# Kernel tuning notes

Hardware: AMD Instinct MI355X
Metric: run time of the kernel (lower is better)

The kernel has to match this reference:

```python
import jax, jax.numpy as jnp
from jax import lax
import numpy as np


def conv2d(x, w, b=None, padding=0, dilation=1, groups=1):
    out = lax.conv_general_dilated(
        x, w, window_strides=(1, 1),
        padding=[(padding, padding), (padding, padding)],
        rhs_dilation=(dilation, dilation),
        dimension_numbers=('NCHW', 'OIHW', 'NCHW'),
        feature_group_count=groups)
    return out if b is None else out + b[None, :, None, None]


def hardswish(x):
    return x * jnp.clip(x + 3.0, 0.0, 6.0) / 6.0


def leaky(x, s):
    return jnp.where(x >= 0, x, s * x)


def bn_eval(x, g, b, eps=1e-5):
    # BatchNorm2d eval mode with running_mean=0, running_var=1
    scale = g * (1.0 / float(np.sqrt(1.0 + eps)))
    return x * scale[None, :, None, None] + b[None, :, None, None]


def deform_dw_conv(x, offset, w):
    # torchvision DeformConv2d, depthwise (groups=C), k=3, stride=1, pad=1, dil=1
    # x [B,C,H,W], offset [B,18,H,W] (y,x interleaved, kernel row-major), w [C,1,3,3]
    B, C, H, W = x.shape
    xf = x.reshape(B, C, H * W)
    yy = jnp.arange(H, dtype=x.dtype)[:, None]
    xx = jnp.arange(W, dtype=x.dtype)[None, :]
    out = jnp.zeros_like(x)
    for k in range(9):
        ky, kx = k // 3 - 1, k % 3 - 1
        py = yy + ky + offset[:, 2 * k]          # [B,H,W]
        px = xx + kx + offset[:, 2 * k + 1]
        y0 = jnp.floor(py)
        x0 = jnp.floor(px)
        wy = py - y0
        wx = px - x0
        y0i = y0.astype(jnp.int32)
        x0i = x0.astype(jnp.int32)
        val = jnp.zeros_like(x)
        for dy, dx, wgt in ((0, 0, (1 - wy) * (1 - wx)), (0, 1, (1 - wy) * wx),
                            (1, 0, wy * (1 - wx)), (1, 1, wy * wx)):
            iy = y0i + dy
            ix = x0i + dx
            valid = (iy >= 0) & (iy < H) & (ix >= 0) & (ix < W)
            idx = (jnp.clip(iy, 0, H - 1) * W + jnp.clip(ix, 0, W - 1)).reshape(B, 1, H * W)
            g = jnp.take_along_axis(xf, idx, axis=2).reshape(B, C, H, W)
            val = val + g * (wgt * valid.astype(x.dtype))[:, None]
        out = out + val * w[:, 0, ky + 1, kx + 1][None, :, None, None]
    return out


def patch_embed(x, off_dw, off_pw, dcn_w, pw_w):
    g = x.shape[1]
    off = conv2d(x, off_dw, padding=1, groups=g)
    off = jnp.clip(conv2d(off, off_pw), -1.0, 1.0)
    y = deform_dw_conv(x, off, dcn_w)
    return hardswish(conv2d(y, pw_w))


def depth_conv(x, dw_w, dw_b, pw_w, pw_b):
    g = x.shape[1]
    return conv2d(conv2d(x, dw_w, dw_b, padding=1, groups=g), pw_w, pw_b)


def cross_attn(hs, ctx, dw_w, dw_b, pw_w, pw_b):
    q = depth_conv(hs, dw_w[0], dw_b[0], pw_w[0], pw_b[0])
    k = depth_conv(ctx, dw_w[1], dw_b[1], pw_w[1], pw_b[1])
    v = depth_conv(ctx, dw_w[2], dw_b[2], pw_w[2], pw_b[2])
    head = q.shape[1] // 8  # num_heads = 8
    qt = q.transpose(0, 2, 1, 3)  # [B,H,C,W]
    kt = k.transpose(0, 2, 1, 3)
    vt = v.transpose(0, 2, 1, 3)
    scores = jnp.einsum('bhcw,bhdw->bhcd', qt, kt) / float(np.sqrt(head))
    probs = jax.nn.softmax(scores, axis=-1)
    o = jnp.einsum('bhcd,bhdw->bhcw', probs, vt)
    return o.transpose(0, 2, 1, 3)  # back to [B,C,H,W]


def dilated_block(x, ws, bs):
    h = x
    for i, d in enumerate((1, 2, 3, 2, 1)):
        h = conv2d(h, ws[i], bs[i], padding=d, dilation=d)
        if i < 4:
            h = leaky(h, 0.01)
    return h + x


def fft_block(h, fd1_w, fd2_w, fd1_g, fd1_bt, fd2_g, fd2_bt, fconv_w):
    Hh, Ww = h.shape[-2], h.shape[-1]
    xf = jnp.fft.rfft2(h)  # norm='backward'
    re, im = jnp.real(xf), jnp.imag(xf)
    mag = jnp.sqrt(re * re + im * im)
    pha = jnp.arctan2(im, re)

    def branch(m, i):
        t = leaky(bn_eval(conv2d(m, fd1_w[i]), fd1_g[i], fd1_bt[i]), 0.1)
        m1 = jnp.concatenate([m, t], 1)          # C+32
        t2 = leaky(bn_eval(conv2d(m1, fd2_w[i]), fd2_g[i], fd2_bt[i]), 0.1)
        m2 = jnp.concatenate([m1, t2], 1)        # C+64
        return conv2d(m2, fconv_w[i])            # back to C

    mag_o = branch(mag, 0)
    pha_o = branch(pha, 1)
    real = mag_o * jnp.cos(pha_o)
    imag = mag_o * jnp.sin(pha_o)
    out = jnp.fft.irfft2(lax.complex(real, imag), s=(Hh, Ww)) + h
    return out, mag_o, pha_o


def scarm_forward(x, ch_off_dw, ch_off_pw, ch_dcn_w, ch_pw,
                  ct_off_dw, ct_off_pw, ct_dcn_w, ct_pw,
                  db_w, db_b, ca_dw_w, ca_dw_b, ca_pw_w, ca_pw_b,
                  convHH_w, convHH_b, fd1_w, fd2_w, fd1_g, fd1_bt,
                  fd2_g, fd2_bt, fconv_w, conv_w, conv_b):
    b = x.shape[0]
    residual = x
    h = patch_embed(x, ch_off_dw, ch_off_pw, ch_dcn_w, ch_pw)  # [B,64,H,W]
    fft_out, mag, pha = fft_block(h, fd1_w, fd2_w, fd1_g, fd1_bt, fd2_g, fd2_bt, fconv_w)
    t = b // 3
    x_HL, x_LH, x_HH = h[:t], h[t:2 * t], h[2 * t:]
    # note: faithful to source, which aliases fft_LH/fft_HH back to x (h)
    fft_HL, fft_LH, fft_HH = fft_out[:t], h[t:2 * t], h[2 * t:]
    x_HH_LH = cross_attn(x_LH, x_HH, ca_dw_w[0], ca_dw_b[0], ca_pw_w[0], ca_pw_b[0])
    x_HH_HL = cross_attn(x_HL, x_HH, ca_dw_w[1], ca_dw_b[1], ca_pw_w[1], ca_pw_b[1])
    f_HH_LH = cross_attn(fft_LH, fft_HH, ca_dw_w[0], ca_dw_b[0], ca_pw_w[0], ca_pw_b[0])
    f_HH_HL = cross_attn(fft_HL, fft_HH, ca_dw_w[1], ca_dw_b[1], ca_pw_w[1], ca_pw_b[1])
    x_HL2 = dilated_block(x_HL, db_w[1], db_b[1])
    x_LH2 = dilated_block(x_LH, db_w[0], db_b[0])
    x_HH2 = dilated_block(conv2d(jnp.concatenate([x_HH_LH, x_HH_HL], 1), convHH_w, convHH_b, padding=1), db_w[2], db_b[2])
    f_HH2 = dilated_block(conv2d(jnp.concatenate([f_HH_LH, f_HH_HL], 1), convHH_w, convHH_b, padding=1), db_w[2], db_b[2])
    out = patch_embed(jnp.concatenate([x_HL2, x_LH2, x_HH2], 0), ct_off_dw, ct_off_pw, ct_dcn_w, ct_pw)
    fftout = patch_embed(jnp.concatenate([fft_HL, fft_LH, f_HH2], 0), ct_off_dw, ct_off_pw, ct_dcn_w, ct_pw)
    out = conv2d(jnp.concatenate([out, fftout], 1), conv_w, conv_b, padding=1)
    return out + residual, mag, pha


def setup_inputs() -> dict:
    key = jax.random.key(0)
    ks = iter(jax.random.split(key, 32))

    def rn(shape, scale):
        return jax.random.normal(next(ks), shape, jnp.float32) * scale

    return {
        'x': rn([12, 3, 128, 128], 1.0),
        'ch_off_dw': rn([3, 1, 3, 3], 0.3), 'ch_off_pw': rn([18, 3, 1, 1], 0.3),
        'ch_dcn_w': rn([3, 1, 3, 3], 0.3), 'ch_pw': rn([64, 3, 1, 1], 0.3),
        'ct_off_dw': rn([64, 1, 3, 3], 0.1), 'ct_off_pw': rn([18, 64, 1, 1], 0.1),
        'ct_dcn_w': rn([64, 1, 3, 3], 0.1), 'ct_pw': rn([3, 64, 1, 1], 0.05),
        'db_w': rn([3, 5, 64, 64, 3, 3], 0.05), 'db_b': rn([3, 5, 64], 0.01),
        'ca_dw_w': rn([2, 3, 64, 1, 3, 3], 0.3), 'ca_dw_b': rn([2, 3, 64], 0.01),
        'ca_pw_w': rn([2, 3, 64, 64, 1, 1], 0.1), 'ca_pw_b': rn([2, 3, 64], 0.01),
        'convHH_w': rn([64, 128, 3, 3], 0.03), 'convHH_b': rn([64], 0.01),
        'fd1_w': rn([2, 32, 64, 1, 1], 0.1), 'fd2_w': rn([2, 32, 96, 1, 1], 0.1),
        'fd1_g': 1.0 + rn([2, 32], 0.1), 'fd1_bt': rn([2, 32], 0.1),
        'fd2_g': 1.0 + rn([2, 32], 0.1), 'fd2_bt': rn([2, 32], 0.1),
        'fconv_w': rn([2, 64, 128, 1, 1], 0.1),
        'conv_w': rn([3, 6, 3, 3], 0.1), 'conv_b': rn([3], 0.01),
    }


def reference(x, ch_off_dw, ch_off_pw, ch_dcn_w, ch_pw,
              ct_off_dw, ct_off_pw, ct_dcn_w, ct_pw,
              db_w, db_b, ca_dw_w, ca_dw_b, ca_pw_w, ca_pw_b,
              convHH_w, convHH_b, fd1_w, fd2_w, fd1_g, fd1_bt,
              fd2_g, fd2_bt, fconv_w, conv_w, conv_b):
    return scarm_forward(x, ch_off_dw, ch_off_pw, ch_dcn_w, ch_pw,
                         ct_off_dw, ct_off_pw, ct_dcn_w, ct_pw,
                         db_w, db_b, ca_dw_w, ca_dw_b, ca_pw_w, ca_pw_b,
                         convHH_w, convHH_b, fd1_w, fd2_w, fd1_g, fd1_bt,
                         fd2_g, fd2_bt, fconv_w, conv_w, conv_b)
```

## Files before the change

kernel.cpp:

```cpp
#include <hip/hip_runtime.h>

namespace {

constexpr int Hn = 128, Wn = 128, HWn = 16384, HWFn = 8320;
constexpr float TWOPI = 6.2831853071795864769f;
constexpr float BN_SCALE = 0.99999500003749968f;

typedef __attribute__((ext_vector_type(8))) short short8;
typedef __attribute__((ext_vector_type(4))) float float4v;

__device__ __forceinline__ short f2bf(float v){
  unsigned u = __float_as_uint(v);
  u += 0x7FFF + ((u >> 16) & 1);
  return (short)(u >> 16);
}
__device__ __forceinline__ float bf2f(unsigned short u){
  return __uint_as_float(((unsigned)u) << 16);
}

__global__ void k_pack(const float* __restrict__ w, unsigned short* __restrict__ o,
                       int Cin, int csz, int n){
  int idx = blockIdx.x*256 + threadIdx.x;
  if (idx >= n) return;
  int ck = idx / csz;
  int i  = idx - ck*csz;
  const float* wp = w + (size_t)ck*csz;
  int j = i & 7, lane = (i>>3)&63, mt = (i>>9)&3, p = i>>11;
  int blk = p/18, r = p - blk*18, tap = r>>1, ks = r&1;
  int co = mt*16 + (lane & 15);
  int ci = blk*64 + ks*32 + ((lane>>4)<<3) + j;
  o[idx] = (unsigned short)f2bf(wp[((size_t)co*Cin + ci)*9 + tap]);
}

__global__ void k_packpw(const float* __restrict__ w, unsigned short* __restrict__ o,
                         int Cout, int MT, int n){
  int i = blockIdx.x*256 + threadIdx.x;
  if (i >= n) return;
  int per = MT << 10;
  int set = i / per;
  int r = i - set*per;
  int j = r & 7, lane = (r>>3)&63, blk = r>>9;
  int ks = blk / MT, mt = blk - ks*MT;
  int co = mt*16 + (lane & 15);
  int ci = ks*32 + ((lane>>4)<<3) + j;
  float v = (co < Cout) ? w[(size_t)set*Cout*64 + co*64 + ci] : 0.f;
  o[i] = (unsigned short)f2bf(v);
}

__global__ void k_wfdc(const float* __restrict__ fd1w, const float* __restrict__ fd2w,
                       const float* __restrict__ fcw,  const float* __restrict__ fd1g,
                       const float* __restrict__ fd2g, float* __restrict__ o){
  int i = blockIdx.x*256 + threadIdx.x;
  if (i >= 26624) return;
  int br = i / 13312, r = i - br*13312;
  float v;
  if (r < 2048){
    int ci = r >> 5, j = r & 31;
    v = fd1w[br*2048 + j*64 + ci] * (fd1g[br*32 + j]*BN_SCALE);
  } else if (r < 5120){
    int rr = r - 2048; int ci = rr >> 5, j = rr & 31;
    v = fd2w[br*3072 + j*96 + ci] * (fd2g[br*32 + j]*BN_SCALE);
  } else {
    int rr = r - 5120; int ci = rr >> 6, j = rr & 63;
    v = fcw[br*8192 + j*128 + ci];
  }
  o[i] = v;
}

__global__ __launch_bounds__(256) void k_fdc(
    const float* __restrict__ in, const float* __restrict__ wT,
    const float* __restrict__ bt1, const float* __restrict__ bt2,
    float* __restrict__ outp){
  __shared__ float tls[32][64];
  __shared__ float uls[32][64];
  int b = blockIdx.x, tile = blockIdx.y;
  int tid = threadIdx.x;
  int lane = tid & 63;
  int kk = __builtin_amdgcn_readfirstlane(tid >> 6);
  const float* ip = in + (size_t)b*64*HWFn + tile*64 + lane;
  {
    float t[8];
    #pragma unroll
    for (int jj=0;jj<8;jj++) t[jj] = bt1[kk*8+jj];
    for (int ci=0; ci<64; ci++){
      float v = ip[(size_t)ci*HWFn];
      const float* w = wT + ci*32 + kk*8;
      #pragma unroll
      for (int jj=0;jj<8;jj++) t[jj] = fmaf(v, w[jj], t[jj]);
    }
    #pragma unroll
    for (int jj=0;jj<8;jj++){
      float a = t[jj];
      tls[kk*8+jj][lane] = (a>=0.f)? a : 0.1f*a;
    }
  }
  __syncthreads();
  {
    float u[8];
    #pragma unroll
    for (int jj=0;jj<8;jj++) u[jj] = bt2[kk*8+jj];
    for (int ci=0; ci<64; ci++){
      float v = ip[(size_t)ci*HWFn];
      const float* w = wT + 2048 + ci*32 + kk*8;
      #pragma unroll
      for (int jj=0;jj<8;jj++) u[jj] = fmaf(v, w[jj], u[jj]);
    }
    for (int ci=0; ci<32; ci++){
      float v = tls[ci][lane];
      const float* w = wT + 2048 + (64+ci)*32 + kk*8;
      #pragma unroll
      for (int jj=0;jj<8;jj++) u[jj] = fmaf(v, w[jj], u[jj]);
    }
    #pragma unroll
    for (int jj=0;jj<8;jj++){
      float a = u[jj];
      uls[kk*8+jj][lane] = (a>=0.f)? a : 0.1f*a;
    }
  }
  __syncthreads();
  float acc[16];
  #pragma unroll
  for (int jj=0;jj<16;jj++) acc[jj] = 0.f;
  for (int ci=0; ci<64; ci++){
    float v = ip[(size_t)ci*HWFn];
    const float* w = wT + 5120 + ci*64 + kk*16;
    #pragma unroll
    for (int jj=0;jj<16;jj++) acc[jj] = fmaf(v, w[jj], acc[jj]);
  }
  for (int ci=0; ci<32; ci++){
    float v = tls[ci][lane];
    const float* w = wT + 5120 + (64+ci)*64 + kk*16;
    #pragma unroll
    for (int jj=0;jj<16;jj++) acc[jj] = fmaf(v, w[jj], acc[jj]);
  }
  for (int ci=0; ci<32; ci++){
    float v = uls[ci][lane];
    const float* w = wT + 5120 + (96+ci)*64 + kk*16;
    #pragma unroll
    for (int jj=0;jj<16;jj++) acc[jj] = fmaf(v, w[jj], acc[jj]);
  }
  float* op = outp + (size_t)b*64*HWFn + tile*64 + lane;
  #pragma unroll
  for (int jj=0;jj<16;jj++)
    op[(size_t)(kk*16+jj)*HWFn] = acc[jj];
}

constexpr int XST = 72;
__global__ __launch_bounds__(256) void k_mconv(
    const float* __restrict__ in, const float* __restrict__ in2,
    const unsigned short* __restrict__ wpk, const float* __restrict__ bias,
    const float* __restrict__ res, float* __restrict__ out,
    int nblk, int dl, int leaky){
  __shared__ short lds[3*134*XST];
  int b = blockIdx.x >> 7, y = blockIdx.x & 127;
  int tid = threadIdx.x;
  int wv = tid >> 6, lane = tid & 63;
  int nq = lane >> 4, nr = lane & 15;
  float4v acc[4][2];
  #pragma unroll
  for (int mt=0; mt<4; mt++)
    #pragma unroll
    for (int nt=0; nt<2; nt++) acc[mt][nt] = (float4v){0.f,0.f,0.f,0.f};

  for (int blk=0; blk<nblk; blk++){
    const float* src = blk ? in2 : in;
    __syncthreads();
    for (int e = tid; e < 3*16*32; e += 256){
      int dy = e >> 9;
      int r  = e & 511;
      int c4 = r >> 5;
      int xx = (r & 31) << 2;
      int yy = y + (dy-1)*dl;
      float4 v0, v1, v2, v3;
      if (yy >= 0 && yy < Hn){
        const float* sp2 = src + (((size_t)b*64 + c4*4)*Hn + yy)*Wn + xx;
        v0 = *(const float4*)(sp2);
        v1 = *(const float4*)(sp2 + HWn);
        v2 = *(const float4*)(sp2 + 2*HWn);
        v3 = *(const float4*)(sp2 + 3*HWn);
      } else {
        v0 = v1 = v2 = v3 = make_float4(0.f,0.f,0.f,0.f);
      }
      #pragma unroll
      for (int j=0; j<4; j++){
        float f0 = (&v0.x)[j], f1 = (&v1.x)[j], f2 = (&v2.x)[j], f3 = (&v3.x)[j];
        unsigned p0 = ((unsigned)(unsigned short)f2bf(f0)) | (((unsigned)(unsigned short)f2bf(f1)) << 16);
        unsigned p1 = ((unsigned)(unsigned short)f2bf(f2)) | (((unsigned)(unsigned short)f2bf(f3)) << 16);
        *(uint2*)&lds[(dy*134 + xx + 3 + j)*XST + c4*4] = make_uint2(p0, p1);
      }
    }
    for (int e = tid; e < 3*16*6; e += 256){
      int dy = e / 96; int r = e - dy*96;
      int c4 = r / 6;  int k = r - c4*6;
      int x = (k < 3) ? k : 128 + k;
      *(uint2*)&lds[(dy*134 + x)*XST + c4*4] = make_uint2(0u, 0u);
    }
    __syncthreads();
    const unsigned short* wb = wpk + (size_t)blk*36864;
    #pragma unroll 3
    for (int tap=0; tap<9; tap++){
      int dy = tap/3, dx = tap - (tap/3)*3;
      #pragma unroll
      for (int ks=0; ks<2; ks++){
        short8 a[4];
        #pragma unroll
        for (int mt=0; mt<4; mt++)
          a[mt] = *(const short8*)(wb + (((size_t)(tap*2+ks)*4+mt)<<9) + ((size_t)lane<<3));
        #pragma unroll
        for (int nt=0; nt<2; nt++){
          int x = wv*32 + nt*16 + nr + (dx-1)*dl + 3;
          short8 bf = *(const short8*)&lds[(dy*134 + x)*XST + ks*32 + nq*8];
          #pragma unroll
          for (int mt=0; mt<4; mt++)
            acc[mt][nt] = __builtin_amdgcn_mfma_f32_16x16x32_bf16(a[mt], bf, acc[mt][nt], 0, 0, 0);
        }
      }
    }
  }
  #pragma unroll
  for (int mt=0; mt<4; mt++)
  #pragma unroll
  for (int nt=0; nt<2; nt++){
    int x = wv*32 + nt*16 + nr;
    #pragma unroll
    for (int r2=0; r2<4; r2++){
      int co = mt*16 + nq*4 + r2;
      float a = acc[mt][nt][r2] + (bias ? bias[co] : 0.f);
      if (leaky) a = (a >= 0.f) ? a : 0.01f*a;
      size_t idx = (((size_t)b*64 + co)*Hn + y)*Wn + x;
      if (res) a += res[idx];
      out[idx] = a;
    }
  }
}

template<int MT>
__global__ __launch_bounds__(256) void k_dwpw(
    const float* __restrict__ in, const float* __restrict__ dww, const float* __restrict__ dwb,
    const unsigned short* __restrict__ pwpk, const float* __restrict__ pwb,
    float* __restrict__ out, int Cout, size_t outb, int post){
  __shared__ short tb[128*72];
  __shared__ float wsm[640];
  int b = blockIdx.x >> 7, y = blockIdx.x & 127;
  int tid = threadIdx.x;
  for (int i = tid; i < 640; i += 256)
    wsm[i] = (i < 576) ? dww[i] : (dwb ? dwb[i-576] : 0.f);
  __syncthreads();
  for (int e = tid; e < 2048; e += 256){
    int ci = e >> 5;
    int xx = (e & 31) << 2;
    const float* ip = in + ((size_t)b*64 + ci)*HWn;
    const float* wp = wsm + ci*9;
    float4 a0 = make_float4(0.f,0.f,0.f,0.f), a1 = a0, a2 = a0;
    float L0=0.f,L1=0.f,L2=0.f,R0=0.f,R1=0.f,R2=0.f;
    if (y > 0){
      const float* r = ip + (y-1)*Wn;
      a0 = *(const float4*)(r + xx);
      if (xx) L0 = r[xx-1];
      if (xx < 124) R0 = r[xx+4];
    }
    {
      const float* r = ip + y*Wn;
      a1 = *(const float4*)(r + xx);
      if (xx) L1 = r[xx-1];
      if (xx < 124) R1 = r[xx+4];
    }
    if (y < Hn-1){
      const float* r = ip + (y+1)*Wn;
      a2 = *(const float4*)(r + xx);
      if (xx) L2 = r[xx-1];
      if (xx < 124) R2 = r[xx+4];
    }
    float bb = wsm[576+ci];
    float o0=bb,o1=bb,o2=bb,o3=bb;
    float w0=wp[0],w1=wp[1],w2=wp[2];
    o0 = fmaf(w0,L0,  fmaf(w1,a0.x, fmaf(w2,a0.y, o0)));
    o1 = fmaf(w0,a0.x,fmaf(w1,a0.y, fmaf(w2,a0.z, o1)));
    o2 = fmaf(w0,a0.y,fmaf(w1,a0.z, fmaf(w2,a0.w, o2)));
    o3 = fmaf(w0,a0.z,fmaf(w1,a0.w, fmaf(w2,R0,   o3)));
    w0=wp[3];w1=wp[4];w2=wp[5];
    o0 = fmaf(w0,L1,  fmaf(w1,a1.x, fmaf(w2,a1.y, o0)));
    o1 = fmaf(w0,a1.x,fmaf(w1,a1.y, fmaf(w2,a1.z, o1)));
    o2 = fmaf(w0,a1.y,fmaf(w1,a1.z, fmaf(w2,a1.w, o2)));
    o3 = fmaf(w0,a1.z,fmaf(w1,a1.w, fmaf(w2,R1,   o3)));
    w0=wp[6];w1=wp[7];w2=wp[8];
    o0 = fmaf(w0,L2,  fmaf(w1,a2.x, fmaf(w2,a2.y, o0)));
    o1 = fmaf(w0,a2.x,fmaf(w1,a2.y, fmaf(w2,a2.z, o1)));
    o2 = fmaf(w0,a2.y,fmaf(w1,a2.z, fmaf(w2,a2.w, o2)));
    o3 = fmaf(w0,a2.z,fmaf(w1,a2.w, fmaf(w2,R2,   o3)));
    short* d = &tb[xx*72 + ci];
    d[0]   = f2bf(o0);
    d[72]  = f2bf(o1);
    d[144] = f2bf(o2);
    d[216] = f2bf(o3);
  }
  __syncthreads();
  int wv = tid>>6, lane = tid&63, nq = lane>>4, nr = lane&15;
  float4v acc[MT][2];
  #pragma unroll
  for (int mt=0; mt<MT; mt++)
    #pragma unroll
    for (int nt=0; nt<2; nt++) acc[mt][nt] = (float4v){0.f,0.f,0.f,0.f};
  #pragma unroll
  for (int ks=0; ks<2; ks++){
    short8 a[MT];
    #pragma unroll
    for (int mt=0; mt<MT; mt++)
      a[mt] = *(const short8*)(pwpk + ((ks*MT+mt)<<9) + (lane<<3));
    #pragma unroll
    for (int nt=0; nt<2; nt++){
      int x = wv*32 + nt*16 + nr;
      short8 bf = *(const short8*)&tb[x*72 + ks*32 + nq*8];
      #pragma unroll
      for (int mt=0; mt<MT; mt++)
        acc[mt][nt] = __builtin_amdgcn_mfma_f32_16x16x32_bf16(a[mt], bf, acc[mt][nt], 0, 0, 0);
    }
  }
  #pragma unroll
  for (int mt=0; mt<MT; mt++)
  #pragma unroll
  for (int nt=0; nt<2; nt++){
    int x = wv*32 + nt*16 + nr;
    #pragma unroll
    for (int r2=0; r2<4; r2++){
      int co = mt*16 + nq*4 + r2;
      if (co < Cout){
        float a = acc[mt][nt][r2] + (pwb ? pwb[co] : 0.f);
        if (post == 1) a = fminf(fmaxf(a, -1.f), 1.f);
        else if (post == 2) a = a*fminf(fmaxf(a+3.f, 0.f), 6.f)*(1.f/6.f);
        out[(size_t)b*outb + (size_t)co*HWn + y*Wn + x] = a;
      }
    }
  }
}

__global__ __launch_bounds__(512) void k_defpw(
    const float* __restrict__ xg, const float* __restrict__ off, const float* __restrict__ dcnw,
    const unsigned short* __restrict__ pwpk, float* __restrict__ out,
    int Cout, size_t outb, int post){
  __shared__ unsigned short xs[5*64*130];
  __shared__ short tb[128*72];
  __shared__ float wsm[576];
  int b = blockIdx.x >> 7, y = blockIdx.x & 127;
  int tid = threadIdx.x;
  int px = tid & 127, sub = tid >> 7;
  for (int i = tid; i < 576; i += 512) wsm[i] = dcnw[i];
  for (int e = tid; e < 10240; e += 512){
    int tr = e >> 11;
    int r  = e & 2047;
    int ci = r >> 5;
    int xx = (r & 31) << 2;
    int gy = min(max(y - 2 + tr, 0), Hn-1);
    float4 v = *(const float4*)&xg[(((size_t)b*64 + ci)*Hn + gy)*Wn + xx];
    unsigned short* d = &xs[(tr*64 + ci)*130 + xx];
    d[0] = (unsigned short)f2bf(v.x);
    d[1] = (unsigned short)f2bf(v.y);
    d[2] = (unsigned short)f2bf(v.z);
    d[3] = (unsigned short)f2bf(v.w);
  }
  const float* op = off + (size_t)b*18*HWn + y*Wn + px;
  int t0[9], t1[9], c0[9], c1[9];
  float w00[9], w01[9], w10[9], w11[9];
  #pragma unroll
  for (int k=0; k<9; k++){
    int ky = k/3 - 1, kx = k - (k/3)*3 - 1;
    float oy = op[(size_t)(2*k)*HWn];
    float ox = op[(size_t)(2*k+1)*HWn];
    float py = (float)(y + ky) + oy;
    float pxx = (float)(px + kx) + ox;
    float fy = floorf(py), fx = floorf(pxx);
    float wy = py - fy, wx = pxx - fx;
    int y0 = (int)fy, x0 = (int)fx;
    float vy0 = (y0 >= 0 && y0 < Hn) ? 1.f : 0.f;
    float vy1 = (y0+1 >= 0 && y0+1 < Hn) ? 1.f : 0.f;
    float vx0 = (x0 >= 0 && x0 < Wn) ? 1.f : 0.f;
    float vx1 = (x0+1 >= 0 && x0+1 < Wn) ? 1.f : 0.f;
    w00[k] = (1.f-wy)*(1.f-wx)*vy0*vx0;
    w01[k] = (1.f-wy)*wx*vy0*vx1;
    w10[k] = wy*(1.f-wx)*vy1*vx0;
    w11[k] = wy*wx*vy1*vx1;
    t0[k] = min(max(min(max(y0,   0), Hn-1) - (y-2), 0), 4);
    t1[k] = min(max(min(max(y0+1, 0), Hn-1) - (y-2), 0), 4);
    c0[k] = min(max(x0,   0), Wn-1);
    c1[k] = min(max(x0+1, 0), Wn-1);
  }
  __syncthreads();
  for (int ci = sub; ci < 64; ci += 4){
    float acc = 0.f;
    #pragma unroll
    for (int k=0; k<9; k++){
      const unsigned short* b0 = &xs[(t0[k]*64 + ci)*130];
      const unsigned short* b1 = &xs[(t1[k]*64 + ci)*130];
      float v = w00[k]*bf2f(b0[c0[k]]) + w01[k]*bf2f(b0[c1[k]])
              + w10[k]*bf2f(b1[c0[k]]) + w11[k]*bf2f(b1[c1[k]]);
      acc = fmaf(v, wsm[ci*9 + k], acc);
    }
    tb[px*72 + ci] = f2bf(acc);
  }
  __syncthreads();
  int wv = tid>>6, lane = tid&63, nq = lane>>4, nr = lane&15;
  float4v acc = (float4v){0.f,0.f,0.f,0.f};
  int x = wv*16 + nr;
  #pragma unroll
  for (int ks=0; ks<2; ks++){
    short8 a = *(const short8*)(pwpk + (ks<<9) + (lane<<3));
    short8 bf = *(const short8*)&tb[x*72 + ks*32 + nq*8];
    acc = __builtin_amdgcn_mfma_f32_16x16x32_bf16(a, bf, acc, 0, 0, 0);
  }
  #pragma unroll
  for (int r2=0; r2<4; r2++){
    int co = nq*4 + r2;
    if (co < Cout){
      float a = acc[r2];
      if (post == 2) a = a*fminf(fmaxf(a+3.f, 0.f), 6.f)*(1.f/6.f);
      out[(size_t)b*outb + (size_t)co*HWn + y*Wn + x] = a;
    }
  }
}

__global__ void k_dw3x3(const float* __restrict__ in, const float* __restrict__ w,
                        const float* __restrict__ bias, float* __restrict__ out, int C){
  int bc = blockIdx.x; int y = blockIdx.y; int x = threadIdx.x;
  int c = bc % C;
  const float* ip = in + (size_t)bc*HWn;
  const float* wp = w + c*9;
  float acc = bias ? bias[c] : 0.f;
  #pragma unroll
  for (int ky=0; ky<3; ky++){
    int yy = y + ky - 1; if (yy < 0 || yy >= Hn) continue;
    #pragma unroll
    for (int kx=0; kx<3; kx++){
      int xx = x + kx - 1; if (xx < 0 || xx >= Wn) continue;
      acc = fmaf(ip[yy*Wn+xx], wp[ky*3+kx], acc);
    }
  }
  out[(size_t)bc*HWn + y*Wn + x] = acc;
}

template<int CT>
__global__ void k_pwt(const float* __restrict__ in, const float* __restrict__ wg,
                      const float* __restrict__ bias, const float* __restrict__ bng,
                      const float* __restrict__ bnb, float* __restrict__ out,
                      int Cin, int Cout, int npix, int inb, int outb, int post, float slope){
  extern __shared__ float wsm[];
  int nt = (Cout + CT - 1)/CT;
  int b = blockIdx.x / nt, t = blockIdx.x - b*nt;
  int co0 = t*CT;
  for (int i = threadIdx.x; i < CT*Cin; i += 256){
    int co = i / Cin;
    wsm[i] = (co0 + co < Cout) ? wg[(size_t)(co0+co)*Cin + (i - co*Cin)] : 0.f;
  }
  __syncthreads();
  int p = blockIdx.y*256 + threadIdx.x;
  if (p >= npix) return;
  const float* ip = in + (size_t)b*inb + p;
  float acc[CT];
  #pragma unroll
  for (int j=0; j<CT; j++) acc[j] = 0.f;
  for (int ci=0; ci<Cin; ci++){
    float v = ip[(size_t)ci*npix];
    #pragma unroll
    for (int j=0; j<CT; j++) acc[j] = fmaf(v, wsm[j*Cin+ci], acc[j]);
  }
  #pragma unroll
  for (int j=0; j<CT; j++){
    int co = co0 + j;
    if (co < Cout){
      float a = acc[j] + (bias ? bias[co] : 0.f);
      if (bng) a = a*(bng[co]*BN_SCALE) + bnb[co];
      if (post == 1) a = fminf(fmaxf(a, -1.f), 1.f);
      else if (post == 2) a = a*fminf(fmaxf(a+3.f, 0.f), 6.f)*(1.f/6.f);
      else if (post == 3) a = (a >= 0.f) ? a : a*slope;
      out[(size_t)b*outb + (size_t)co*npix + p] = a;
    }
  }
}

__global__ void k_deform(const float* __restrict__ x, const float* __restrict__ off,
                         const float* __restrict__ w, float* __restrict__ out, int C){
  int bc = blockIdx.x; int b = bc / C; int c = bc - b*C;
  int y = blockIdx.y; int x0 = threadIdx.x;
  const float* xp = x + (size_t)bc*HWn;
  const float* op = off + (size_t)b*18*HWn + y*Wn + x0;
  const float* wp = w + c*9;
  float acc = 0.f;
  #pragma unroll
  for (int k=0; k<9; k++){
    int ky = k/3 - 1, kx = k - (k/3)*3 - 1;
    float oy = op[(size_t)(2*k)*HWn];
    float ox = op[(size_t)(2*k+1)*HWn];
    float py = (float)y + (float)ky + oy;
    float px = (float)x0 + (float)kx + ox;
    float fy = floorf(py), fx = floorf(px);
    float wy = py - fy, wx = px - fx;
    int y0 = (int)fy, xx0 = (int)fx;
    float val = 0.f;
    #pragma unroll
    for (int dy=0; dy<2; dy++){
      int iy = y0 + dy; if (iy < 0 || iy >= Hn) continue;
      float wyv = dy ? wy : (1.f - wy);
      #pragma unroll
      for (int dx=0; dx<2; dx++){
        int ix = xx0 + dx; if (ix < 0 || ix >= Wn) continue;
        float wxv = dx ? wx : (1.f - wx);
        val = fmaf(xp[iy*Wn+ix], wyv*wxv, val);
      }
    }
    acc = fmaf(val, wp[k], acc);
  }
  out[(size_t)bc*HWn + y*Wn + x0] = acc;
}

__global__ void k_conv3x3s(const float* __restrict__ in, const float* __restrict__ wgt,
                           const float* __restrict__ bias, const float* __restrict__ res,
                           float* __restrict__ out, int Cin, int Cout){
  int g = blockIdx.x;
  int b = g / Cout; int o0 = g - b*Cout;
  int y = blockIdx.y, x = threadIdx.x;
  float acc = bias ? bias[o0] : 0.f;
  for (int ci=0; ci<Cin; ci++){
    const float* iip = in + ((size_t)b*Cin + ci)*HWn;
    const float* wp = wgt + ((size_t)o0*Cin + ci)*9;
    #pragma unroll
    for (int ky=0; ky<3; ky++){
      int yy = y + ky - 1; if (yy < 0 || yy >= Hn) continue;
      #pragma unroll
      for (int kx=0; kx<3; kx++){
        int xx = x + kx - 1; if (xx < 0 || xx >= Wn) continue;
        acc = fmaf(iip[yy*Wn+xx], wp[ky*3+kx], acc);
      }
    }
  }
  size_t idx = ((size_t)b*Cout + o0)*HWn + y*Wn + x;
  if (res) acc += res[idx];
  out[idx] = acc;
}

__global__ __launch_bounds__(256) void k_attn(
    const float* __restrict__ q, const float* __restrict__ k,
    const float* __restrict__ v, float* __restrict__ o){
  __shared__ float qs[64][129];
  __shared__ float ks[64][129];
  __shared__ float vs[64][129];
  __shared__ float ps[64][66];
  int bh = blockIdx.x; int b = bh >> 7, h = bh & 127;
  size_t base = ((size_t)b*64*128 + h)*128;
  int tid = threadIdx.x;
  for (int e = tid; e < 8192; e += 256){
    int c = e >> 7, w = e & 127;
    size_t g = base + (size_t)c*HWn + w;
    qs[c][w] = q[g]; ks[c][w] = k[g]; vs[c][w] = v[g];
  }
  __syncthreads();
  {
    int c0 = (tid >> 4) << 2, d0 = (tid & 15) << 2;
    float acc[4][4];
    #pragma unroll
    for (int a=0; a<4; a++)
      #pragma unroll
      for (int bb=0; bb<4; bb++) acc[a][bb] = 0.f;
    for (int i=0; i<128; i++){
      float qv[4], kv[4];
      #pragma unroll
      for (int a=0; a<4; a++){ qv[a] = qs[c0+a][i]; kv[a] = ks[d0+a][i]; }
      #pragma unroll
      for (int a=0; a<4; a++)
        #pragma unroll
        for (int bb=0; bb<4; bb++) acc[a][bb] = fmaf(qv[a], kv[bb], acc[a][bb]);
    }
    #pragma unroll
    for (int a=0; a<4; a++)
      #pragma unroll
      for (int bb=0; bb<4; bb++)
        ps[c0+a][d0+bb] = acc[a][bb] * 0.35355339059327373f;
  }
  __syncthreads();
  {
    int wv = tid >> 6, lane = tid & 63;
    for (int it=0; it<16; it++){
      int row = wv*16 + it;
      float vv = ps[row][lane];
      float m = vv;
      #pragma unroll
      for (int off=32; off; off>>=1) m = fmaxf(m, __shfl_xor(m, off));
      float e = expf(vv - m);
      float s = e;
      #pragma unroll
      for (int off=32; off; off>>=1) s += __shfl_xor(s, off);
      ps[row][lane] = e / s;
    }
  }
  __syncthreads();
  {
    int c0 = (tid >> 4) << 2, w0 = (tid & 15) << 3;
    float acc[4][8];
    #pragma unroll
    for (int a=0; a<4; a++)
      #pragma unroll
      for (int j=0; j<8; j++) acc[a][j] = 0.f;
    for (int d=0; d<64; d++){
      float pv[4], vv[8];
      #pragma unroll
      for (int a=0; a<4; a++) pv[a] = ps[c0+a][d];
      #pragma unroll
      for (int j=0; j<8; j++) vv[j] = vs[d][w0+j];
      #pragma unroll
      for (int a=0; a<4; a++)
        #pragma unroll
        for (int j=0; j<8; j++) acc[a][j] = fmaf(pv[a], vv[j], acc[a][j]);
    }
    #pragma unroll
    for (int a=0; a<4; a++)
      #pragma unroll
      for (int j=0; j<8; j++)
        o[base + (size_t)(c0+a)*HWn + w0 + j] = acc[a][j];
  }
}

__device__ __forceinline__ float2 cmul(float2 a, float2 b){
  return make_float2(a.x*b.x - a.y*b.y, a.x*b.y + a.y*b.x);
}

__device__ __forceinline__ void wfft4(float2* z, const float2* twl, int l){
  #pragma unroll
  for (int q=0; q<2; q++){
    float dx = z[2*q].x - z[2*q+1].x, dy = z[2*q].y - z[2*q+1].y;
    z[2*q].x += z[2*q+1].x; z[2*q].y += z[2*q+1].y;
    z[2*q+1] = cmul(make_float2(dx, dy), twl[6]);
  }
  #pragma unroll
  for (int s = 5; s >= 0; --s){
    int h = 1 << s;
    bool up = (l & h) != 0;
    float2 w = twl[s];
    #pragma unroll
    for (int q=0; q<4; q++){
      float ox = __shfl_xor(z[q].x, h), oy = __shfl_xor(z[q].y, h);
      float sx = up ? ox - z[q].x : z[q].x + ox;
      float sy = up ? oy - z[q].y : z[q].y + oy;
      float2 t = cmul(make_float2(sx, sy), w);
      z[q].x = up ? t.x : sx;  z[q].y = up ? t.y : sy;
    }
  }
}

__device__ __forceinline__ void wreorder(float2 z0, float2 z1, float2& n0, float2& n1, int l){
  int a = (int)(__brev((unsigned)(l >> 1)) >> 26);
  float p0x = __shfl(z0.x, a),   p0y = __shfl(z0.y, a);
  float p1x = __shfl(z1.x, a),   p1y = __shfl(z1.y, a);
  float q0x = __shfl(z0.x, a+1), q0y = __shfl(z0.y, a+1);
  float q1x = __shfl(z1.x, a+1), q1y = __shfl(z1.y, a+1);
  bool odd = (l & 1) != 0;
  n0 = odd ? make_float2(p1x, p1y) : make_float2(p0x, p0y);
  n1 = odd ? make_float2(q1x, q1y) : make_float2(q0x, q0y);
}

__global__ __launch_bounds__(256) void k_fft2(
    const float* __restrict__ x, float* __restrict__ mag, float* __restrict__ pha){
  __shared__ float spr[8320];
  __shared__ float spi[8320];
  int img = blockIdx.x;
  int tid = threadIdx.x;
  int wv = tid >> 6, l = tid & 63;
  float2 twl[7];
  #pragma unroll
  for (int s = 0; s < 7; ++s){
    int jh = (l & ((1 << s) - 1)) << (6 - s);
    float sv, cv; sincosf(-TWOPI * (float)jh * (1.f/128.f), &sv, &cv);
    twl[s] = make_float2(cv, sv);
  }
  const float* xp = x + (size_t)img*HWn;
  for (int f = wv; f < 32; f += 4){
    int fB = f + 32;
    float2 z[4];
    {
      const float* a0 = xp + (2*f)*Wn;  const float* a1 = a0 + Wn;
      const float* b0 = xp + (2*fB)*Wn; const float* b1 = b0 + Wn;
      z[0] = make_float2(a0[l],      a1[l]);
      z[1] = make_float2(a0[64 + l], a1[64 + l]);
      z[2] = make_float2(b0[l],      b1[l]);
      z[3] = make_float2(b0[64 + l], b1[64 + l]);
    }
    wfft4(z, twl, l);
    #pragma unroll
    for (int q=0; q<2; q++){
      int ff = q ? fB : f;
      float2 n0, n1; wreorder(z[2*q], z[2*q+1], n0, n1, l);
      float zhx = __shfl(n1.x, (64 - l) & 63);
      float zhy = __shfl(n1.y, (64 - l) & 63);
      float2 Zn = (l == 0) ? n0 : make_float2(zhx, zhy);
      int iA = (2*ff)*65 + l, iB = (2*ff+1)*65 + l;
      spr[iA] = 0.5f*(n0.x + Zn.x);  spi[iA] = 0.5f*(n0.y - Zn.y);
      spr[iB] = 0.5f*(n0.y + Zn.y);  spi[iB] = 0.5f*(Zn.x - n0.x);
      if (l == 0){
        spr[(2*ff)*65 + 64]   = n1.x;  spi[(2*ff)*65 + 64]   = 0.f;
        spr[(2*ff+1)*65 + 64] = n1.y;  spi[(2*ff+1)*65 + 64] = 0.f;
      }
    }
  }
  __syncthreads();
  for (int c = wv; c < 33; c += 4){
    int cB = c + 33;
    bool h2 = cB < 65;
    int cB_s = h2 ? cB : c;
    float2 z[4];
    z[0] = make_float2(spr[l*65 + c],        spi[l*65 + c]);
    z[1] = make_float2(spr[(64 + l)*65 + c], spi[(64 + l)*65 + c]);
    z[2] = make_float2(spr[l*65 + cB_s],        spi[l*65 + cB_s]);
    z[3] = make_float2(spr[(64 + l)*65 + cB_s], spi[(64 + l)*65 + cB_s]);
    wfft4(z, twl, l);
    {
      float2 n0, n1; wreorder(z[0], z[1], n0, n1, l);
      spr[l*65 + c]        = sqrtf(n0.x*n0.x + n0.y*n0.y);
      spi[l*65 + c]        = atan2f(n0.y, n0.x);
      spr[(64 + l)*65 + c] = sqrtf(n1.x*n1.x + n1.y*n1.y);
      spi[(64 + l)*65 + c] = atan2f(n1.y, n1.x);
    }
    if (h2){
      float2 n0, n1; wreorder(z[2], z[3], n0, n1, l);
      spr[l*65 + cB]        = sqrtf(n0.x*n0.x + n0.y*n0.y);
      spi[l*65 + cB]        = atan2f(n0.y, n0.x);
      spr[(64 + l)*65 + cB] = sqrtf(n1.x*n1.x + n1.y*n1.y);
      spi[(64 + l)*65 + cB] = atan2f(n1.y, n1.x);
    }
  }
  __syncthreads();
  float* mp = mag + (size_t)img*HWFn;
  float* pp = pha + (size_t)img*HWFn;
  for (int i = tid; i < 8320; i += 256){
    mp[i] = spr[i]; pp[i] = spi[i];
  }
}

__global__ __launch_bounds__(256) void k_ifft2(
    const float* __restrict__ mo, const float* __restrict__ po,
    const float* __restrict__ hsrc, float* __restrict__ outp){
  __shared__ float spr[8320];
  __shared__ float spi[8320];
  int img = blockIdx.x;
  int tid = threadIdx.x;
  int wv = tid >> 6, l = tid & 63;
  float2 twl[7];
  #pragma unroll
  for (int s = 0; s < 7; ++s){
    int jh = (l & ((1 << s) - 1)) << (6 - s);
    float sv, cv; sincosf(TWOPI * (float)jh * (1.f/128.f), &sv, &cv);
    twl[s] = make_float2(cv, sv);
  }
  const float* mp = mo + (size_t)img*HWFn;
  const float* pp = po + (size_t)img*HWFn;
  for (int i = tid; i < 8320; i += 256){
    float m = mp[i], p = pp[i];
    float sv, cv; sincosf(p, &sv, &cv);
    spr[i] = m*cv; spi[i] = m*sv;
  }
  __syncthreads();
  for (int c = wv; c < 33; c += 4){
    int cB = c + 33;
    bool h2 = cB < 65;
    int cB_s = h2 ? cB : c;
    float2 z[4];
    z[0] = make_float2(spr[l*65 + c],        spi[l*65 + c]);
    z[1] = make_float2(spr[(64 + l)*65 + c], spi[(64 + l)*65 + c]);
    z[2] = make_float2(spr[l*65 + cB_s],        spi[l*65 + cB_s]);
    z[3] = make_float2(spr[(64 + l)*65 + cB_s], spi[(64 + l)*65 + cB_s]);
    wfft4(z, twl, l);
    {
      float2 n0, n1; wreorder(z[0], z[1], n0, n1, l);
      spr[l*65 + c] = n0.x;        spi[l*65 + c] = n0.y;
      spr[(64 + l)*65 + c] = n1.x; spi[(64 + l)*65 + c] = n1.y;
    }
    if (h2){
      float2 n0, n1; wreorder(z[2], z[3], n0, n1, l);
      spr[l*65 + cB] = n0.x;        spi[l*65 + cB] = n0.y;
      spr[(64 + l)*65 + cB] = n1.x; spi[(64 + l)*65 + cB] = n1.y;
    }
  }
  __syncthreads();
  const float scl = 1.f/16384.f;
  for (int f = wv; f < 32; f += 4){
    int fB = f + 32;
    float2 z[4];
    #pragma unroll
    for (int q=0; q<2; q++){
      int ff = q ? fB : f;
      int iA = (2*ff)*65 + l, iB = (2*ff+1)*65 + l;
      float2 A  = make_float2(spr[iA], spi[iA]);
      float2 Bv = make_float2(spr[iB], spi[iB]);
      if (l == 0){ A.y = 0.f; Bv.y = 0.f; }
      z[2*q] = make_float2(A.x - Bv.y, A.y + Bv.x);
      int lm = 64 - l;
      float2 Am = make_float2(spr[(2*ff)*65 + lm],   spi[(2*ff)*65 + lm]);
      float2 Bm = make_float2(spr[(2*ff+1)*65 + lm], spi[(2*ff+1)*65 + lm]);
      z[2*q+1] = (l == 0) ? make_float2(Am.x, Bm.x)
                          : make_float2(Am.x + Bm.y, Bm.x - Am.y);
    }
    wfft4(z, twl, l);
    #pragma unroll
    for (int q=0; q<2; q++){
      int ff = q ? fB : f;
      float2 n0, n1; wreorder(z[2*q], z[2*q+1], n0, n1, l);
      size_t g0 = (size_t)img*HWn + (size_t)(2*ff)*Wn + l;
      size_t g1 = g0 + Wn;
      outp[g0]      = n0.x*scl + hsrc[g0];
      outp[g0 + 64] = n1.x*scl + hsrc[g0 + 64];
      outp[g1]      = n0.y*scl + hsrc[g1];
      outp[g1 + 64] = n1.y*scl + hsrc[g1 + 64];
    }
  }
}

}

extern "C" void kernel_launch(void* const* d_in, const int* in_sizes, int n_in,
                              void* d_out, int out_size, void* d_ws, size_t ws_size,
                              hipStream_t stream){
  const float *xf   =(const float*)d_in[0],  *chodw=(const float*)d_in[1],
              *chopw=(const float*)d_in[2],  *chdcn=(const float*)d_in[3],
              *chpw =(const float*)d_in[4],  *ctodw=(const float*)d_in[5],
              *ctopw=(const float*)d_in[6],  *ctdcn=(const float*)d_in[7],
              *ctpw =(const float*)d_in[8],  *dbw  =(const float*)d_in[9],
              *dbb  =(const float*)d_in[10], *cadw =(const float*)d_in[11],
              *cadb =(const float*)d_in[12], *capw =(const float*)d_in[13],
              *capb =(const float*)d_in[14], *hhw  =(const float*)d_in[15],
              *hhb  =(const float*)d_in[16], *fd1w =(const float*)d_in[17],
              *fd2w =(const float*)d_in[18], *fd1g =(const float*)d_in[19],
              *fd1bt=(const float*)d_in[20], *fd2g =(const float*)d_in[21],
              *fd2bt=(const float*)d_in[22], *fcw  =(const float*)d_in[23],
              *cw   =(const float*)d_in[24], *cb   =(const float*)d_in[25];

  constexpr size_t M = 1048576;
  float* ws = (float*)d_ws;
  float* h     = ws;
  float* fftHL = ws + 12*M;
  float* cat6  = ws + 16*M;
  unsigned short* wpkDB = (unsigned short*)(cat6 + 1179648);
  unsigned short* wpkHH = wpkDB + 552960;
  float* wfdc = (float*)(wpkHH + 73728);
  float* P = cat6 + 1179648 + 313344 + 26624;

  const int NB = (ws_size >= 266018816ull) ? 4 : 1;
  const size_t S = (size_t)NB*M;
  float* kb  = P;        float* vb  = P + S;   float* qb  = P + 2*S;
  float* qsl = P + 3*S;
  float* aA  = P + 4*S;  float* aB  = P + 5*S;
  float* aC  = P + 6*S;  float* hh1 = P + 7*S; float* sA  = P + 8*S;
  float* sB  = P + 9*S;  float* dbuf= P + 10*S;
  float* X   = P + 11*S;
  unsigned short* pwpkCA = (unsigned short*)qsl;
  unsigned short* pwpkTO = pwpkCA + 24576;
  unsigned short* pwpkTP = pwpkTO + 2048;
  float* dwb3 = P; float* offb12 = P + 589824; float* yb3 = P + 4128768;

  float* out = (float*)d_out;
  float* out0 = out;
  float* out1 = out + 589824;
  float* out2 = out + 589824 + 6389760;

  auto PW = [&](const float* in, const float* wg, const float* bi, const float* g, const float* bt,
                float* o, int B, int Ci, int Co, int npix, int inb, int outb, int post, float slope){
    int py = (npix + 255)/256;
    if (Co > 32){
      k_pwt<32><<<dim3(B*2, py), 256, 32*Ci*4, stream>>>(in, wg, bi, g, bt, o, Ci, Co, npix, inb, outb, post, slope);
    } else if (Co > 18){
      k_pwt<32><<<dim3(B, py), 256, 32*Ci*4, stream>>>(in, wg, bi, g, bt, o, Ci, Co, npix, inb, outb, post, slope);
    } else if (Co > 3){
      k_pwt<18><<<dim3(B, py), 256, 18*Ci*4, stream>>>(in, wg, bi, g, bt, o, Ci, Co, npix, inb, outb, post, slope);
    } else {
      k_pwt<3><<<dim3(B, py), 256, 3*Ci*4, stream>>>(in, wg, bi, g, bt, o, Ci, Co, npix, inb, outb, post, slope);
    }
  };
  auto MCONV = [&](const float* in, const float* in2, const unsigned short* wp, const float* bi,
                   const float* res, float* o, int B, int nblk, int dl, int lk){
    k_mconv<<<B*128, 256, 0, stream>>>(in, in2, wp, bi, res, o, nblk, dl, lk);
  };
  auto DILm = [&](const float* in, int set, const float* bset, int B){
    const unsigned short* w5 = wpkDB + (size_t)set*5*36864;
    MCONV(in, nullptr, w5,          bset,      nullptr, sA,   B, 1, 1, 1);
    MCONV(sA, nullptr, w5+36864,    bset+64,   nullptr, sB,   B, 1, 2, 1);
    MCONV(sB, nullptr, w5+2*36864,  bset+128,  nullptr, sA,   B, 1, 3, 1);
    MCONV(sA, nullptr, w5+3*36864,  bset+192,  nullptr, sB,   B, 1, 2, 1);
    MCONV(sB, nullptr, w5+4*36864,  bset+256,  in,      dbuf, B, 1, 1, 0);
  };
  auto DCONVm = [&](const float* in, int idx, float* o, int B){
    k_dwpw<4><<<B*128, 256, 0, stream>>>(in, cadw + idx*576, cadb + idx*64,
        pwpkCA + (size_t)idx*4096, capb + idx*64, o, 64, (size_t)64*HWn, 0);
  };
  auto ATTNm = [&](const float* qsrc, int qidx, float* o, int B){
    DCONVm(qsrc, qidx, qb, B);
    k_attn<<<B*128, 256, 0, stream>>>(qb, kb, vb, o);
  };
  auto PEMBEDm = [&](const float* in, float* outSlice, int B){
    k_dwpw<2><<<B*128, 256, 0, stream>>>(in, ctodw, nullptr, pwpkTO, nullptr,
        X, 18, (size_t)18*HWn, 1);
    k_defpw<<<B*128, 512, 0, stream>>>(in, X, ctdcn, pwpkTP, outSlice, 3, (size_t)6*HWn, 2);
  };

  k_pack<<<(552960 + 255)/256, 256, 0, stream>>>(dbw, wpkDB, 64, 36864, 552960);
  k_pack<<<288, 256, 0, stream>>>(hhw, wpkHH, 128, 73728, 73728);
  k_wfdc<<<104, 256, 0, stream>>>(fd1w, fd2w, fcw, fd1g, fd2g, wfdc);

  k_dw3x3<<<dim3(36, Hn), 128, 0, stream>>>(xf, chodw, nullptr, dwb3, 3);
  PW(dwb3, chopw, nullptr, nullptr, nullptr, offb12, 12, 3, 18, HWn, 3*HWn, 18*HWn, 1, 0.f);
  k_deform<<<dim3(36, Hn), 128, 0, stream>>>(xf, offb12, chdcn, yb3, 3);
  PW(yb3, chpw, nullptr, nullptr, nullptr, h, 12, 3, 64, HWn, 3*HWn, 64*HWn, 2, 0.f);

  if (NB == 4){
    float* mB = P;
    float* pB = P + 6389760;
    k_fft2<<<768, 256, 0, stream>>>(h, mB, pB);
    k_fdc<<<dim3(12, 130), 256, 0, stream>>>(mB, wfdc,         fd1bt,      fd2bt,      out1);
    k_fdc<<<dim3(12, 130), 256, 0, stream>>>(pB, wfdc + 13312, fd1bt + 32, fd2bt + 32, out2);
    k_ifft2<<<256, 256, 0, stream>>>(out1, out2, h, fftHL);
  } else {
    float* mB = P;
    float* pB = P + 2129920;
    for (int c=0; c<3; c++){
      const float* hsrc = h + (size_t)c*4*M;
      float* o1 = out1 + (size_t)c*2129920;
      float* o2 = out2 + (size_t)c*2129920;
      k_fft2<<<256, 256, 0, stream>>>(hsrc, mB, pB);
      k_fdc<<<dim3(4, 130), 256, 0, stream>>>(mB, wfdc,         fd1bt,      fd2bt,      o1);
      k_fdc<<<dim3(4, 130), 256, 0, stream>>>(pB, wfdc + 13312, fd1bt + 32, fd2bt + 32, o2);
      if (c == 0)
        k_ifft2<<<256, 256, 0, stream>>>(out1, out2, h, fftHL);
    }
  }

  k_packpw<<<96, 256, 0, stream>>>(capw,  pwpkCA, 64, 4, 24576);
  k_packpw<<<8,  256, 0, stream>>>(ctopw, pwpkTO, 18, 2, 2048);
  k_packpw<<<4,  256, 0, stream>>>(ctpw,  pwpkTP, 3,  1, 1024);

  for (int g0=0; g0<4; g0+=NB){
    const float* hHL = h + (size_t)g0*M;
    const float* hLH = h + (size_t)(4+g0)*M;
    const float* hHH = h + (size_t)(8+g0)*M;
    const float* fHL = fftHL + (size_t)g0*M;
    DCONVm(hHH, 1, kb, NB);
    DCONVm(hHH, 2, vb, NB);
    ATTNm(hLH, 0, aA, NB);
    DCONVm(hHH, 4, kb, NB);
    DCONVm(hHH, 5, vb, NB);
    ATTNm(hHL, 3, aB, NB);
    ATTNm(fHL, 3, aC, NB);
    MCONV(aA, aB, wpkHH, hhb, nullptr, hh1, NB, 2, 1, 0);
    DILm(hh1, 2, dbb + 2*320, NB);
    PEMBEDm(dbuf, cat6 + (size_t)((8+g0)*6)*HWn, NB);
    MCONV(aA, aC, wpkHH, hhb, nullptr, hh1, NB, 2, 1, 0);
    DILm(hh1, 2, dbb + 2*320, NB);
    PEMBEDm(dbuf, cat6 + (size_t)((8+g0)*6+3)*HWn, NB);
    DILm(hHL, 1, dbb + 320, NB);
    PEMBEDm(dbuf, cat6 + (size_t)(g0*6)*HWn, NB);
    DILm(hLH, 0, dbb, NB);
    PEMBEDm(dbuf, cat6 + (size_t)((4+g0)*6)*HWn, NB);
    PEMBEDm(fHL, cat6 + (size_t)(g0*6+3)*HWn, NB);
    PEMBEDm(hLH, cat6 + (size_t)((4+g0)*6+3)*HWn, NB);
  }

  k_conv3x3s<<<dim3(36, Hn), 128, 0, stream>>>(cat6, cw, cb, xf, out0, 6, 3);
}
```

Measured before the change: 1.578 ms.

## Compute two dilated output rows per mconv block; widen FFT blocks to 512 threads

Result: slower. 1.675 ms (+6.1%).

```diff
diff --git a/kernel.cpp b/kernel.cpp
--- a/kernel.cpp
+++ b/kernel.cpp
@@ -151,26 +151,31 @@
     const unsigned short* __restrict__ wpk, const float* __restrict__ bias,
     const float* __restrict__ res, float* __restrict__ out,
     int nblk, int dl, int leaky){
-  __shared__ short lds[3*134*XST];
-  int b = blockIdx.x >> 7, y = blockIdx.x & 127;
+  __shared__ short lds[4*134*XST];
+  int b = blockIdx.x;
+  int p = blockIdx.y;
+  int g = p / dl, i = p - g*dl;
+  int ya = g*2*dl + i;
   int tid = threadIdx.x;
   int wv = tid >> 6, lane = tid & 63;
   int nq = lane >> 4, nr = lane & 15;
-  float4v acc[4][2];
-  #pragma unroll
-  for (int mt=0; mt<4; mt++)
-    #pragma unroll
-    for (int nt=0; nt<2; nt++) acc[mt][nt] = (float4v){0.f,0.f,0.f,0.f};
+  float4v acc[2][4][2];
+  #pragma unroll
+  for (int rr=0; rr<2; rr++)
+    #pragma unroll
+    for (int mt=0; mt<4; mt++)
+      #pragma unroll
+      for (int nt=0; nt<2; nt++) acc[rr][mt][nt] = (float4v){0.f,0.f,0.f,0.f};
 
   for (int blk=0; blk<nblk; blk++){
     const float* src = blk ? in2 : in;
     __syncthreads();
-    for (int e = tid; e < 3*16*32; e += 256){
-      int dy = e >> 9;
+    for (int e = tid; e < 4*16*32; e += 256){
+      int s  = e >> 9;
       int r  = e & 511;
       int c4 = r >> 5;
       int xx = (r & 31) << 2;
-      int yy = y + (dy-1)*dl;
+      int yy = ya + (s-1)*dl;
       float4 v0, v1, v2, v3;
       if (yy >= 0 && yy < Hn){
         const float* sp2 = src + (((size_t)b*64 + c4*4)*Hn + yy)*Wn + xx;
@@ -186,14 +191,14 @@
         float f0 = (&v0.x)[j], f1 = (&v1.x)[j], f2 = (&v2.x)[j], f3 = (&v3.x)[j];
         unsigned p0 = ((unsigned)(unsigned short)f2bf(f0)) | (((unsigned)(unsigned short)f2bf(f1)) << 16);
         unsigned p1 = ((unsigned)(unsigned short)f2bf(f2)) | (((unsigned)(unsigned short)f2bf(f3)) << 16);
-        *(uint2*)&lds[(dy*134 + xx + 3 + j)*XST + c4*4] = make_uint2(p0, p1);
+        *(uint2*)&lds[(s*134 + xx + 3 + j)*XST + c4*4] = make_uint2(p0, p1);
       }
     }
-    for (int e = tid; e < 3*16*6; e += 256){
-      int dy = e / 96; int r = e - dy*96;
+    for (int e = tid; e < 4*16*6; e += 256){
+      int s = e / 96; int r = e - s*96;
       int c4 = r / 6;  int k = r - c4*6;
       int x = (k < 3) ? k : 128 + k;
-      *(uint2*)&lds[(dy*134 + x)*XST + c4*4] = make_uint2(0u, 0u);
+      *(uint2*)&lds[(s*134 + x)*XST + c4*4] = make_uint2(0u, 0u);
     }
     __syncthreads();
     const unsigned short* wb = wpk + (size_t)blk*36864;
@@ -207,29 +212,37 @@
         for (int mt=0; mt<4; mt++)
           a[mt] = *(const short8*)(wb + (((size_t)(tap*2+ks)*4+mt)<<9) + ((size_t)lane<<3));
         #pragma unroll
-        for (int nt=0; nt<2; nt++){
-          int x = wv*32 + nt*16 + nr + (dx-1)*dl + 3;
-          short8 bf = *(const short8*)&lds[(dy*134 + x)*XST + ks*32 + nq*8];
+        for (int rr=0; rr<2; rr++){
           #pragma unroll
-          for (int mt=0; mt<4; mt++)
-            acc[mt][nt] = __builtin_amdgcn_mfma_f32_16x16x32_bf16(a[mt], bf, acc[mt][nt], 0, 0, 0);
+          for (int nt=0; nt<2; nt++){
+            int x = wv*32 + nt*16 + nr + (dx-1)*dl + 3;
+            short8 bf = *(const short8*)&lds[((dy+rr)*134 + x)*XST + ks*32 + nq*8];
+            #pragma unroll
+            for (int mt=0; mt<4; mt++)
+              acc[rr][mt][nt] = __builtin_amdgcn_mfma_f32_16x16x32_bf16(a[mt], bf, acc[rr][mt][nt], 0, 0, 0);
+          }
         }
       }
     }
   }
   #pragma unroll
-  for (int mt=0; mt<4; mt++)
-  #pragma unroll
-  for (int nt=0; nt<2; nt++){
-    int x = wv*32 + nt*16 + nr;
-    #pragma unroll
-    for (int r2=0; r2<4; r2++){
-      int co = mt*16 + nq*4 + r2;
-      float a = acc[mt][nt][r2] + (bias ? bias[co] : 0.f);
-      if (leaky) a = (a >= 0.f) ? a : 0.01f*a;
-      size_t idx = (((size_t)b*64 + co)*Hn + y)*Wn + x;
-      if (res) a += res[idx];
-      out[idx] = a;
+  for (int rr=0; rr<2; rr++){
+    int y = ya + rr*dl;
+    if (y >= Hn) continue;
+    #pragma unroll
+    for (int mt=0; mt<4; mt++)
+    #pragma unroll
+    for (int nt=0; nt<2; nt++){
+      int x = wv*32 + nt*16 + nr;
+      #pragma unroll
+      for (int r2=0; r2<4; r2++){
+        int co = mt*16 + nq*4 + r2;
+        float a = acc[rr][mt][nt][r2] + (bias ? bias[co] : 0.f);
+        if (leaky) a = (a >= 0.f) ? a : 0.01f*a;
+        size_t idx = (((size_t)b*64 + co)*Hn + y)*Wn + x;
+        if (res) a += res[idx];
+        out[idx] = a;
+      }
     }
   }
 }
@@ -655,7 +668,7 @@
   n1 = odd ? make_float2(q1x, q1y) : make_float2(q0x, q0y);
 }
 
-__global__ __launch_bounds__(256) void k_fft2(
+__global__ __launch_bounds__(512) void k_fft2(
     const float* __restrict__ x, float* __restrict__ mag, float* __restrict__ pha){
   __shared__ float spr[8320];
   __shared__ float spi[8320];
@@ -670,7 +683,7 @@
     twl[s] = make_float2(cv, sv);
   }
   const float* xp = x + (size_t)img*HWn;
-  for (int f = wv; f < 32; f += 4){
+  for (int f = wv; f < 32; f += 8){
     int fB = f + 32;
     float2 z[4];
     {
@@ -699,7 +712,7 @@
     }
   }
   __syncthreads();
-  for (int c = wv; c < 33; c += 4){
+  for (int c = wv; c < 33; c += 8){
     int cB = c + 33;
     bool h2 = cB < 65;
     int cB_s = h2 ? cB : c;
@@ -727,12 +740,12 @@
   __syncthreads();
   float* mp = mag + (size_t)img*HWFn;
   float* pp = pha + (size_t)img*HWFn;
-  for (int i = tid; i < 8320; i += 256){
+  for (int i = tid; i < 8320; i += 512){
     mp[i] = spr[i]; pp[i] = spi[i];
   }
 }
 
-__global__ __launch_bounds__(256) void k_ifft2(
+__global__ __launch_bounds__(512) void k_ifft2(
     const float* __restrict__ mo, const float* __restrict__ po,
     const float* __restrict__ hsrc, float* __restrict__ outp){
   __shared__ float spr[8320];
@@ -749,13 +762,13 @@
   }
   const float* mp = mo + (size_t)img*HWFn;
   const float* pp = po + (size_t)img*HWFn;
-  for (int i = tid; i < 8320; i += 256){
+  for (int i = tid; i < 8320; i += 512){
     float m = mp[i], p = pp[i];
     float sv, cv; sincosf(p, &sv, &cv);
     spr[i] = m*cv; spi[i] = m*sv;
   }
   __syncthreads();
-  for (int c = wv; c < 33; c += 4){
+  for (int c = wv; c < 33; c += 8){
     int cB = c + 33;
     bool h2 = cB < 65;
     int cB_s = h2 ? cB : c;
@@ -778,7 +791,7 @@
   }
   __syncthreads();
   const float scl = 1.f/16384.f;
-  for (int f = wv; f < 32; f += 4){
+  for (int f = wv; f < 32; f += 8){
     int fB = f + 32;
     float2 z[4];
     #pragma unroll
@@ -872,7 +885,8 @@
   };
   auto MCONV = [&](const float* in, const float* in2, const unsigned short* wp, const float* bi,
                    const float* res, float* o, int B, int nblk, int dl, int lk){
-    k_mconv<<<B*128, 256, 0, stream>>>(in, in2, wp, bi, res, o, nblk, dl, lk);
+    int npairs = (dl == 3) ? 66 : 64;
+    k_mconv<<<dim3(B, npairs), 256, 0, stream>>>(in, in2, wp, bi, res, o, nblk, dl, lk);
   };
   auto DILm = [&](const float* in, int set, const float* bset, int B){
     const unsigned short* w5 = wpkDB + (size_t)set*5*36864;
@@ -908,10 +922,10 @@
   if (NB == 4){
     float* mB = P;
     float* pB = P + 6389760;
-    k_fft2<<<768, 256, 0, stream>>>(h, mB, pB);
+    k_fft2<<<768, 512, 0, stream>>>(h, mB, pB);
     k_fdc<<<dim3(12, 130), 256, 0, stream>>>(mB, wfdc,         fd1bt,      fd2bt,      out1);
     k_fdc<<<dim3(12, 130), 256, 0, stream>>>(pB, wfdc + 13312, fd1bt + 32, fd2bt + 32, out2);
-    k_ifft2<<<256, 256, 0, stream>>>(out1, out2, h, fftHL);
+    k_ifft2<<<256, 512, 0, stream>>>(out1, out2, h, fftHL);
   } else {
     float* mB = P;
     float* pB = P + 2129920;
@@ -919,11 +933,11 @@
       const float* hsrc = h + (size_t)c*4*M;
       float* o1 = out1 + (size_t)c*2129920;
       float* o2 = out2 + (size_t)c*2129920;
-      k_fft2<<<256, 256, 0, stream>>>(hsrc, mB, pB);
+      k_fft2<<<256, 512, 0, stream>>>(hsrc, mB, pB);
       k_fdc<<<dim3(4, 130), 256, 0, stream>>>(mB, wfdc,         fd1bt,      fd2bt,      o1);
       k_fdc<<<dim3(4, 130), 256, 0, stream>>>(pB, wfdc + 13312, fd1bt + 32, fd2bt + 32, o2);
       if (c == 0)
-        k_ifft2<<<256, 256, 0, stream>>>(out1, out2, h, fftHL);
+        k_ifft2<<<256, 512, 0, stream>>>(out1, out2, h, fftHL);
     }
   }
 
```
